# Kernel optimization log

Hardware: AMD Instinct MI355X
Metric: run time of the kernel (lower is better)

Reference implementation:

```python
import jax, jax.numpy as jnp
import numpy as np

B, N, K = 4, 32768, 16
IN_DIM, HID, OUT_DIM = 32, 64, 32
N_DIM = 2
KIN = 2 * N_DIM + OUT_DIM  # 36
KH = 64
EPS = 1e-5


def _gelu(x):
    return jax.nn.gelu(x, approximate=False)  # torch F.gelu default (erf)


def setup_inputs() -> dict:
    key = jax.random.key(0)
    ks = jax.random.split(key, 16)
    s = lambda fan_in: 1.0 / np.sqrt(fan_in)
    return {
        "inp": jax.random.normal(ks[0], (B, N, IN_DIM), jnp.float32),
        "input_grid": jax.random.uniform(ks[1], (N, N_DIM), jnp.float32),
        "output_grid": jax.random.uniform(ks[2], (N, N_DIM), jnp.float32),
        "neighbor_idx": jax.random.randint(ks[3], (N, K), 0, N, jnp.int32),
        # pointwise projection MLP: in_dim -> hid -> out_dim, GELU between
        "Wp1": jax.random.normal(ks[4], (IN_DIM, HID), jnp.float32) * s(IN_DIM),
        "bp1": jnp.zeros((HID,), jnp.float32),
        "Wp2": jax.random.normal(ks[5], (HID, OUT_DIM), jnp.float32) * s(HID),
        "bp2": jnp.zeros((OUT_DIM,), jnp.float32),
        # per-edge kernel MLP: [2*n_dim+out_dim, 64, 64, out_dim], GELU between
        "Wk1": jax.random.normal(ks[6], (KIN, KH), jnp.float32) * s(KIN),
        "bk1": jnp.zeros((KH,), jnp.float32),
        "Wk2": jax.random.normal(ks[7], (KH, KH), jnp.float32) * s(KH),
        "bk2": jnp.zeros((KH,), jnp.float32),
        "Wk3": jax.random.normal(ks[8], (KH, OUT_DIM), jnp.float32) * s(KH),
        "bk3": jnp.zeros((OUT_DIM,), jnp.float32),
        # LayerNorm
        "ln_gamma": jnp.ones((OUT_DIM,), jnp.float32),
        "ln_beta": jnp.zeros((OUT_DIM,), jnp.float32),
    }


def reference(inp, input_grid, output_grid, neighbor_idx,
              Wp1, bp1, Wp2, bp2, Wk1, bk1, Wk2, bk2, Wk3, bk3,
              ln_gamma, ln_beta):
    # pointwise projection MLP
    x = _gelu(jnp.einsum('bnc,ch->bnh', inp, Wp1) + bp1)
    x = jnp.einsum('bnh,ho->bno', x, Wp2) + bp2  # (B, N, OUT_DIM)

    # neighbor gather (fixed K neighbors per output point)
    f_y = x[:, neighbor_idx, :]                      # (B, N, K, C)
    y_pos = input_grid[neighbor_idx]                 # (N, K, n_dim)
    x_pos = jnp.broadcast_to(output_grid[:, None, :], (N, K, N_DIM))
    pos_feat = jnp.concatenate([y_pos, x_pos], axis=-1)          # (N, K, 2*n_dim)
    agg = jnp.concatenate(
        [jnp.broadcast_to(pos_feat[None], (x.shape[0], N, K, 2 * N_DIM)), f_y],
        axis=-1)                                      # (B, N, K, KIN)

    # nonlinear kernel MLP k(x, y, f(y))
    h = _gelu(jnp.einsum('bnkc,ch->bnkh', agg, Wk1) + bk1)
    h = _gelu(jnp.einsum('bnkh,hg->bnkg', h, Wk2) + bk2)
    k_out = jnp.einsum('bnkg,go->bnko', h, Wk3) + bk3  # (B, N, K, OUT_DIM)

    # mean-aggregate over neighbors (integral transform)
    out = jnp.mean(k_out, axis=2)                      # (B, N, OUT_DIM)

    # residual (shapes match) + LayerNorm over channels
    out = out + x
    mu = jnp.mean(out, axis=-1, keepdims=True)
    var = jnp.mean((out - mu) ** 2, axis=-1, keepdims=True)
    out = (out - mu) * jax.lax.rsqrt(var + EPS) * ln_gamma + ln_beta
    return out
```

## Files before the change

kernel.cpp:

```cpp
#include <hip/hip_runtime.h>
#include <hip/hip_bf16.h>

#define BB 4
#define NN 32768
#define KKN 16
#define IN_DIM 32
#define HID 64
#define OUT_DIM 32
#define KH 64
#define WS 88
#define TOT (BB * NN)
#define NWAVES 8192
#define GTAB_N 4096

typedef __bf16 bf16;
typedef float f32x4 __attribute__((ext_vector_type(4)));
typedef bf16 bf16x8 __attribute__((ext_vector_type(8)));
typedef bf16 bf16x4 __attribute__((ext_vector_type(4)));

__device__ __forceinline__ float gelu_f(float x) {
    float x2 = x * x;
    float t  = x * fmaf(0.10294358f, x2, 2.3022082f);
    float E  = __builtin_amdgcn_exp2f(t);
    float r  = __builtin_amdgcn_rcpf(E + 1.0f);
    return fmaf(-x, r, x);
}

template <int CTRL>
__device__ __forceinline__ float dppadd(float v) {
    union { float f; int i; } u, r;
    u.f = v;
    r.i = __builtin_amdgcn_update_dpp(0, u.i, CTRL, 0xf, 0xf, true);
    return v + r.f;
}
__device__ __forceinline__ float rowsum16(float v) {
    v = dppadd<0xB1>(v);
    v = dppadd<0x4E>(v);
    v = dppadd<0x124>(v);
    v = dppadd<0x128>(v);
    return v;
}

__global__ __launch_bounds__(256) void point_mlp_kernel(
    const float* __restrict__ inp, const float* __restrict__ Wp1,
    const float* __restrict__ bp1, const float* __restrict__ Wp2,
    const float* __restrict__ bp2, bf16* __restrict__ xbf)
{
    __shared__ __align__(16) bf16 hb[4][16 * WS];
    const int tid = threadIdx.x, w = tid >> 6, lane = tid & 63;
    const int q = lane >> 4, nl = lane & 15;

    bf16x8 w1f[4];
    #pragma unroll
    for (int nb = 0; nb < 4; nb++)
        #pragma unroll
        for (int j = 0; j < 8; j++)
            w1f[nb][j] = (bf16)Wp1[(q * 8 + j) * HID + nb * 16 + nl];
    bf16x8 w2f[2][2];
    #pragma unroll
    for (int nb = 0; nb < 2; nb++)
        #pragma unroll
        for (int c = 0; c < 2; c++)
            #pragma unroll
            for (int j = 0; j < 8; j++) {
                int k = c * 32 + q * 8 + j, kp = ((k & 3) << 4) | (k >> 2);
                w2f[nb][c][j] = (bf16)Wp2[kp * OUT_DIM + nb * 16 + nl];
            }
    float b1v[4], b2v[2];
    #pragma unroll
    for (int nb = 0; nb < 4; nb++) b1v[nb] = bp1[nb * 16 + nl];
    b2v[0] = bp2[nl]; b2v[1] = bp2[16 + nl];

    const int gw = blockIdx.x * 4 + w;
    const int nw = gridDim.x * 4;

    for (int t = gw; t < TOT / 16; t += nw) {
        const int R = t * 16;
        const float* ap = inp + (size_t)(R + nl) * IN_DIM + q * 8;
        float4 av0 = *(const float4*)ap, av1 = *(const float4*)(ap + 4);
        bf16x8 af;
        af[0] = (bf16)av0.x; af[1] = (bf16)av0.y; af[2] = (bf16)av0.z; af[3] = (bf16)av0.w;
        af[4] = (bf16)av1.x; af[5] = (bf16)av1.y; af[6] = (bf16)av1.z; af[7] = (bf16)av1.w;

        f32x4 acc[4];
        #pragma unroll
        for (int nb = 0; nb < 4; nb++)
            acc[nb] = (f32x4){b1v[nb], b1v[nb], b1v[nb], b1v[nb]};
        #pragma unroll
        for (int nb = 0; nb < 4; nb++)
            acc[nb] = __builtin_amdgcn_mfma_f32_16x16x32_bf16(af, w1f[nb], acc[nb], 0, 0, 0);

        #pragma unroll
        for (int r = 0; r < 4; r++) {
            bf16x4 hv;
            #pragma unroll
            for (int nb = 0; nb < 4; nb++) hv[nb] = (bf16)gelu_f(acc[nb][r]);
            *(bf16x4*)&hb[w][(q * 4 + r) * WS + nl * 4] = hv;
        }
        bf16x8 a0 = *(const bf16x8*)&hb[w][nl * WS + q * 8];
        bf16x8 a1 = *(const bf16x8*)&hb[w][nl * WS + 32 + q * 8];
        f32x4 a2[2];
        #pragma unroll
        for (int nb = 0; nb < 2; nb++) {
            a2[nb] = (f32x4){b2v[nb], b2v[nb], b2v[nb], b2v[nb]};
            a2[nb] = __builtin_amdgcn_mfma_f32_16x16x32_bf16(a0, w2f[nb][0], a2[nb], 0, 0, 0);
            a2[nb] = __builtin_amdgcn_mfma_f32_16x16x32_bf16(a1, w2f[nb][1], a2[nb], 0, 0, 0);
        }
        #pragma unroll
        for (int r = 0; r < 4; r++)
            #pragma unroll
            for (int nb = 0; nb < 2; nb++)
                xbf[(size_t)(R + q * 4 + r) * OUT_DIM + nb * 16 + nl] = (bf16)a2[nb][r];
    }
}

__global__ __launch_bounds__(256) void gnn_edge_kernel(
    const bf16*  __restrict__ xbf,
    const float* __restrict__ igrid, const float* __restrict__ ogrid,
    const int*   __restrict__ nbi,
    const float* __restrict__ Wk1, const float* __restrict__ bk1,
    const float* __restrict__ Wk2, const float* __restrict__ bk2,
    const float* __restrict__ Wk3, const float* __restrict__ bk3,
    const float* __restrict__ gma, const float* __restrict__ bta,
    float* __restrict__ out)
{
    __shared__ __align__(16) bf16 tile[8][16 * WS];
    __shared__ __align__(16) bf16 gtab[GTAB_N];

    const int tid = threadIdx.x, w = tid >> 6, lane = tid & 63;
    const int q = lane >> 4, nl = lane & 15;
    bf16* __restrict__ TA = tile[w * 2];
    bf16* __restrict__ TB = tile[w * 2 + 1];

    for (int i = tid; i < GTAB_N; i += 256) {
        float x = (float)i * 0.0078125f - 16.0f;
        gtab[i] = (bf16)(0.5f * x * (1.0f + erff(x * 0.70710678f)));
    }

    bf16x8 w1f[4][2], w2f[4][2], w3f[2][2];
    #pragma unroll
    for (int nb = 0; nb < 4; nb++) {
        #pragma unroll
        for (int j = 0; j < 8; j++) {
            w1f[nb][0][j] = (bf16)Wk1[(4 + q * 8 + j) * KH + nb * 16 + nl];
            float v1 = 0.0f;
            if (j < 4 && q == 0) v1 = Wk1[j * KH + nb * 16 + nl];
            w1f[nb][1][j] = (bf16)v1;
        }
        #pragma unroll
        for (int c = 0; c < 2; c++)
            #pragma unroll
            for (int j = 0; j < 8; j++) {
                int k = c * 32 + q * 8 + j, kp = ((k & 3) << 4) | (k >> 2);
                w2f[nb][c][j] = (bf16)Wk2[kp * KH + nb * 16 + nl];
            }
    }
    #pragma unroll
    for (int nb = 0; nb < 2; nb++)
        #pragma unroll
        for (int c = 0; c < 2; c++)
            #pragma unroll
            for (int j = 0; j < 8; j++) {
                int k = c * 32 + q * 8 + j, kp = ((k & 3) << 4) | (k >> 2);
                w3f[nb][c][j] = (bf16)Wk3[kp * OUT_DIM + nb * 16 + nl];
            }

    float b1v[4], b2v[4], b3v[2];
    #pragma unroll
    for (int nb = 0; nb < 4; nb++) { b1v[nb] = bk1[nb * 16 + nl]; b2v[nb] = bk2[nb * 16 + nl]; }
    b3v[0] = bk3[nl]; b3v[1] = bk3[16 + nl];
    const float g0 = gma[nl], g1 = gma[16 + nl], be0 = bta[nl], be1 = bta[16 + nl];

    const int gw = blockIdx.x * 4 + w;
    const int e = lane >> 2, part = lane & 3;

    {
        const bf16x8 zf = {(bf16)0.f,(bf16)0.f,(bf16)0.f,(bf16)0.f,(bf16)0.f,(bf16)0.f,(bf16)0.f,(bf16)0.f};
        for (int i = lane * 8; i < 16 * WS; i += 64 * 8) { *(bf16x8*)&TA[i] = zf; *(bf16x8*)&TB[i] = zf; }
    }
    __syncthreads();

    #define GLUT(x) gtab[(unsigned)fminf(fmaxf(fmaf((x), 128.0f, 2048.5f), 0.0f), 4095.0f)]

    int tA = gw, tB = gw + NWAVES;
    int nA = nbi[(tA & (NN - 1)) * KKN + e];
    int nB = nbi[(tB & (NN - 1)) * KKN + e];
    uint4 fyA = ((const uint4*)(xbf + ((size_t)((tA >> 15) * NN + nA)) * OUT_DIM))[part];
    uint4 fyB = ((const uint4*)(xbf + ((size_t)((tB >> 15) * NN + nB)) * OUT_DIM))[part];
    float2 ipA, opA, ipB, opB;
    if (part == 0) {
        ipA = ((const float2*)igrid)[nA]; opA = ((const float2*)ogrid)[tA & (NN - 1)];
        ipB = ((const float2*)igrid)[nB]; opB = ((const float2*)ogrid)[tB & (NN - 1)];
    }
    bf16 xA0 = xbf[(size_t)tA * OUT_DIM + nl],      xA1 = xbf[(size_t)tA * OUT_DIM + 16 + nl];
    bf16 xB0 = xbf[(size_t)tB * OUT_DIM + nl],      xB1 = xbf[(size_t)tB * OUT_DIM + 16 + nl];

    #pragma unroll 1
    for (int it = 0; it < TOT / (2 * NWAVES); ++it) {
        *(uint4*)&TA[e * WS + part * 8] = fyA;
        *(uint4*)&TB[e * WS + part * 8] = fyB;
        if (part == 0) {
            bf16x4 pA = {(bf16)ipA.x, (bf16)ipA.y, (bf16)opA.x, (bf16)opA.y};
            bf16x4 pB = {(bf16)ipB.x, (bf16)ipB.y, (bf16)opB.x, (bf16)opB.y};
            *(bf16x4*)&TA[e * WS + 32] = pA;
            *(bf16x4*)&TB[e * WS + 32] = pB;
        }
        const float rA0 = (float)xA0, rA1 = (float)xA1, rB0 = (float)xB0, rB1 = (float)xB1;

        const int tA2 = (tA + 2 * NWAVES) & (TOT - 1);
        const int tB2 = tA2 + NWAVES;
        const int nA2 = nbi[(tA2 & (NN - 1)) * KKN + e];
        const int nB2 = nbi[(tB2 & (NN - 1)) * KKN + e];

        bf16x8 aA0 = *(const bf16x8*)&TA[nl * WS + q * 8];
        bf16x8 aA1 = *(const bf16x8*)&TA[nl * WS + 32 + q * 8];
        bf16x8 aB0 = *(const bf16x8*)&TB[nl * WS + q * 8];
        bf16x8 aB1 = *(const bf16x8*)&TB[nl * WS + 32 + q * 8];
        f32x4 cA[4], cB[4];
        #pragma unroll
        for (int nb = 0; nb < 4; nb++) {
            cA[nb] = (f32x4){b1v[nb], b1v[nb], b1v[nb], b1v[nb]};
            cB[nb] = (f32x4){b1v[nb], b1v[nb], b1v[nb], b1v[nb]};
        }
        #pragma unroll
        for (int nb = 0; nb < 4; nb++) {
            cA[nb] = __builtin_amdgcn_mfma_f32_16x16x32_bf16(aA0, w1f[nb][0], cA[nb], 0, 0, 0);
            cB[nb] = __builtin_amdgcn_mfma_f32_16x16x32_bf16(aB0, w1f[nb][0], cB[nb], 0, 0, 0);
            cA[nb] = __builtin_amdgcn_mfma_f32_16x16x32_bf16(aA1, w1f[nb][1], cA[nb], 0, 0, 0);
            cB[nb] = __builtin_amdgcn_mfma_f32_16x16x32_bf16(aB1, w1f[nb][1], cB[nb], 0, 0, 0);
        }
        #pragma unroll
        for (int r = 0; r < 4; r++) {
            bf16x4 hA, hB;
            hA[0] = GLUT(cA[0][r]);          hB[0] = GLUT(cB[0][r]);
            hA[1] = GLUT(cA[1][r]);          hB[1] = GLUT(cB[1][r]);
            hA[2] = (bf16)gelu_f(cA[2][r]);  hB[2] = (bf16)gelu_f(cB[2][r]);
            hA[3] = (bf16)gelu_f(cA[3][r]);  hB[3] = (bf16)gelu_f(cB[3][r]);
            *(bf16x4*)&TA[(q * 4 + r) * WS + nl * 4] = hA;
            *(bf16x4*)&TB[(q * 4 + r) * WS + nl * 4] = hB;
        }

        uint4 fyA2 = ((const uint4*)(xbf + ((size_t)((tA2 >> 15) * NN + nA2)) * OUT_DIM))[part];
        uint4 fyB2 = ((const uint4*)(xbf + ((size_t)((tB2 >> 15) * NN + nB2)) * OUT_DIM))[part];
        float2 ipA2, opA2, ipB2, opB2;
        if (part == 0) {
            ipA2 = ((const float2*)igrid)[nA2]; opA2 = ((const float2*)ogrid)[tA2 & (NN - 1)];
            ipB2 = ((const float2*)igrid)[nB2]; opB2 = ((const float2*)ogrid)[tB2 & (NN - 1)];
        }
        bf16 xA0n = xbf[(size_t)tA2 * OUT_DIM + nl],  xA1n = xbf[(size_t)tA2 * OUT_DIM + 16 + nl];
        bf16 xB0n = xbf[(size_t)tB2 * OUT_DIM + nl],  xB1n = xbf[(size_t)tB2 * OUT_DIM + 16 + nl];

        aA0 = *(const bf16x8*)&TA[nl * WS + q * 8];
        aA1 = *(const bf16x8*)&TA[nl * WS + 32 + q * 8];
        aB0 = *(const bf16x8*)&TB[nl * WS + q * 8];
        aB1 = *(const bf16x8*)&TB[nl * WS + 32 + q * 8];
        #pragma unroll
        for (int nb = 0; nb < 4; nb++) {
            cA[nb] = (f32x4){b2v[nb], b2v[nb], b2v[nb], b2v[nb]};
            cB[nb] = (f32x4){b2v[nb], b2v[nb], b2v[nb], b2v[nb]};
        }
        #pragma unroll
        for (int nb = 0; nb < 4; nb++) {
            cA[nb] = __builtin_amdgcn_mfma_f32_16x16x32_bf16(aA0, w2f[nb][0], cA[nb], 0, 0, 0);
            cB[nb] = __builtin_amdgcn_mfma_f32_16x16x32_bf16(aB0, w2f[nb][0], cB[nb], 0, 0, 0);
            cA[nb] = __builtin_amdgcn_mfma_f32_16x16x32_bf16(aA1, w2f[nb][1], cA[nb], 0, 0, 0);
            cB[nb] = __builtin_amdgcn_mfma_f32_16x16x32_bf16(aB1, w2f[nb][1], cB[nb], 0, 0, 0);
        }
        #pragma unroll
        for (int r = 0; r < 4; r++) {
            bf16x4 hA, hB;
            hA[0] = GLUT(cA[0][r]);          hB[0] = GLUT(cB[0][r]);
            hA[1] = GLUT(cA[1][r]);          hB[1] = GLUT(cB[1][r]);
            hA[2] = (bf16)gelu_f(cA[2][r]);  hB[2] = (bf16)gelu_f(cB[2][r]);
            hA[3] = (bf16)gelu_f(cA[3][r]);  hB[3] = (bf16)gelu_f(cB[3][r]);
            *(bf16x4*)&TA[(q * 4 + r) * WS + nl * 4] = hA;
            *(bf16x4*)&TB[(q * 4 + r) * WS + nl * 4] = hB;
        }

        aA0 = *(const bf16x8*)&TA[nl * WS + q * 8];
        aA1 = *(const bf16x8*)&TA[nl * WS + 32 + q * 8];
        aB0 = *(const bf16x8*)&TB[nl * WS + q * 8];
        aB1 = *(const bf16x8*)&TB[nl * WS + 32 + q * 8];
        f32x4 dA[2], dB[2];
        #pragma unroll
        for (int nb = 0; nb < 2; nb++) {
            dA[nb] = (f32x4){0.f, 0.f, 0.f, 0.f};
            dB[nb] = (f32x4){0.f, 0.f, 0.f, 0.f};
            dA[nb] = __builtin_amdgcn_mfma_f32_16x16x32_bf16(aA0, w3f[nb][0], dA[nb], 0, 0, 0);
            dB[nb] = __builtin_amdgcn_mfma_f32_16x16x32_bf16(aB0, w3f[nb][0], dB[nb], 0, 0, 0);
            dA[nb] = __builtin_amdgcn_mfma_f32_16x16x32_bf16(aA1, w3f[nb][1], dA[nb], 0, 0, 0);
            dB[nb] = __builtin_amdgcn_mfma_f32_16x16x32_bf16(aB1, w3f[nb][1], dB[nb], 0, 0, 0);
        }

        {
            float s0 = dA[0][0] + dA[0][1] + dA[0][2] + dA[0][3];
            float s1 = dA[1][0] + dA[1][1] + dA[1][2] + dA[1][3];
            float u0 = dB[0][0] + dB[0][1] + dB[0][2] + dB[0][3];
            float u1 = dB[1][0] + dB[1][1] + dB[1][2] + dB[1][3];
            s0 += __shfl_xor(s0, 16, 64); s0 += __shfl_xor(s0, 32, 64);
            s1 += __shfl_xor(s1, 16, 64); s1 += __shfl_xor(s1, 32, 64);
            u0 += __shfl_xor(u0, 16, 64); u0 += __shfl_xor(u0, 32, 64);
            u1 += __shfl_xor(u1, 16, 64); u1 += __shfl_xor(u1, 32, 64);

            float oA0 = s0 * 0.0625f + b3v[0] + rA0;
            float oA1 = s1 * 0.0625f + b3v[1] + rA1;
            float oB0 = u0 * 0.0625f + b3v[0] + rB0;
            float oB1 = u1 * 0.0625f + b3v[1] + rB1;

            float mA = rowsum16(oA0 + oA1) * (1.0f / 32.0f);
            float mB = rowsum16(oB0 + oB1) * (1.0f / 32.0f);
            float dA0 = oA0 - mA, dA1 = oA1 - mA, dB0 = oB0 - mB, dB1 = oB1 - mB;
            float vA = rowsum16(dA0 * dA0 + dA1 * dA1) * (1.0f / 32.0f);
            float vB = rowsum16(dB0 * dB0 + dB1 * dB1) * (1.0f / 32.0f);
            float rsA = rsqrtf(vA + 1e-5f);
            float rsB = rsqrtf(vB + 1e-5f);

            if (q == 0) {
                float* oa = out + (size_t)tA * OUT_DIM;
                float* ob = out + (size_t)tB * OUT_DIM;
                oa[nl]      = fmaf(dA0 * rsA, g0, be0);
                oa[16 + nl] = fmaf(dA1 * rsA, g1, be1);
                ob[nl]      = fmaf(dB0 * rsB, g0, be0);
                ob[16 + nl] = fmaf(dB1 * rsB, g1, be1);
            }
        }

        tA = tA2; tB = tB2;
        fyA = fyA2; fyB = fyB2;
        ipA = ipA2; opA = opA2; ipB = ipB2; opB = opB2;
        xA0 = xA0n; xA1 = xA1n; xB0 = xB0n; xB1 = xB1n;
    }
    #undef GLUT
}

extern "C" void kernel_launch(void* const* d_in, const int* in_sizes, int n_in,
                              void* d_out, int out_size, void* d_ws, size_t ws_size,
                              hipStream_t stream) {
    const float* inp   = (const float*)d_in[0];
    const float* igrid = (const float*)d_in[1];
    const float* ogrid = (const float*)d_in[2];
    const int*   nbi   = (const int*)d_in[3];
    const float* Wp1   = (const float*)d_in[4];
    const float* bp1   = (const float*)d_in[5];
    const float* Wp2   = (const float*)d_in[6];
    const float* bp2   = (const float*)d_in[7];
    const float* Wk1   = (const float*)d_in[8];
    const float* bk1   = (const float*)d_in[9];
    const float* Wk2   = (const float*)d_in[10];
    const float* bk2   = (const float*)d_in[11];
    const float* Wk3   = (const float*)d_in[12];
    const float* bk3   = (const float*)d_in[13];
    const float* gma   = (const float*)d_in[14];
    const float* bta   = (const float*)d_in[15];
    float* out = (float*)d_out;
    bf16* xbf = (bf16*)d_ws;

    point_mlp_kernel<<<1024, 256, 0, stream>>>(inp, Wp1, bp1, Wp2, bp2, xbf);
    gnn_edge_kernel<<<2048, 256, 0, stream>>>(xbf, igrid, ogrid, nbi,
                                              Wk1, bk1, Wk2, bk2, Wk3, bk3,
                                              gma, bta, out);
}
```

Measured before the change: 214.4 us.

## Switch to fp16 MFMA with packed fp16 polynomial GELU and fewer waves

Changes the working precision from bf16 to fp16 for the activations and MFMA operands. It replaces the GELU lookup table and the exp/rcp GELU with a packed-fp16 polynomial, evaluated two values at a time on the clamped input. It also drops the shared-memory GELU table and its __syncthreads, halves the edge-kernel grid (NWAVES 4096, 1024 blocks) and adds a launch-bounds occupancy hint. This should cut VALU work in the GELU-heavy inner loop, at the risk of accuracy loss from the fp16 range and the polynomial approximation.

```diff
diff --git a/kernel.cpp b/kernel.cpp
--- a/kernel.cpp
+++ b/kernel.cpp
@@ -1,5 +1,4 @@
 #include <hip/hip_runtime.h>
-#include <hip/hip_bf16.h>
 
 #define BB 4
 #define NN 32768
@@ -10,20 +9,37 @@
 #define KH 64
 #define WS 88
 #define TOT (BB * NN)
-#define NWAVES 8192
-#define GTAB_N 4096
-
-typedef __bf16 bf16;
+#define NWAVES 4096
+
+typedef _Float16 f16;
+typedef f16 f16x2 __attribute__((ext_vector_type(2)));
+typedef f16 f16x4 __attribute__((ext_vector_type(4)));
+typedef f16 f16x8 __attribute__((ext_vector_type(8)));
 typedef float f32x4 __attribute__((ext_vector_type(4)));
-typedef bf16 bf16x8 __attribute__((ext_vector_type(8)));
-typedef bf16 bf16x4 __attribute__((ext_vector_type(4)));
-
-__device__ __forceinline__ float gelu_f(float x) {
-    float x2 = x * x;
-    float t  = x * fmaf(0.10294358f, x2, 2.3022082f);
-    float E  = __builtin_amdgcn_exp2f(t);
-    float r  = __builtin_amdgcn_rcpf(E + 1.0f);
-    return fmaf(-x, r, x);
+typedef __fp16 hf16x2 __attribute__((ext_vector_type(2)));
+
+#define H2(c) ((f16x2){(f16)(c), (f16)(c)})
+
+__device__ __forceinline__ f16x2 cvt2(float a, float b) {
+    hf16x2 r = __builtin_amdgcn_cvt_pkrtz(a, b);
+    return __builtin_bit_cast(f16x2, r);
+}
+
+__device__ __forceinline__ f16x2 gelu2(float a, float b) {
+    f16x2 x  = cvt2(a, b);
+    f16x2 s  = __builtin_elementwise_min(
+                   __builtin_elementwise_max(x, H2(-3.5f)), H2(3.5f));
+    f16x2 s4 = s * H2(0.25f);
+    f16x2 t  = s4 * s4;
+    f16x2 g  = H2(-1.0110344f);
+    g = g * t + H2( 2.85016064f);
+    g = g * t + H2(-3.40439040f);
+    g = g * t + H2( 2.32402432f);
+    g = g * t + H2(-1.04974080f);
+    g = g * t + H2( 0.39879504f);
+    f16x2 f  = s * g;
+    f16x2 hx = x * H2(0.5f);
+    return x * f + hx;
 }
 
 template <int CTRL>
@@ -44,19 +60,19 @@
 __global__ __launch_bounds__(256) void point_mlp_kernel(
     const float* __restrict__ inp, const float* __restrict__ Wp1,
     const float* __restrict__ bp1, const float* __restrict__ Wp2,
-    const float* __restrict__ bp2, bf16* __restrict__ xbf)
+    const float* __restrict__ bp2, f16* __restrict__ xhf)
 {
-    __shared__ __align__(16) bf16 hb[4][16 * WS];
+    __shared__ __align__(16) f16 hb[4][16 * WS];
     const int tid = threadIdx.x, w = tid >> 6, lane = tid & 63;
     const int q = lane >> 4, nl = lane & 15;
 
-    bf16x8 w1f[4];
+    f16x8 w1f[4];
     #pragma unroll
     for (int nb = 0; nb < 4; nb++)
         #pragma unroll
         for (int j = 0; j < 8; j++)
-            w1f[nb][j] = (bf16)Wp1[(q * 8 + j) * HID + nb * 16 + nl];
-    bf16x8 w2f[2][2];
+            w1f[nb][j] = (f16)Wp1[(q * 8 + j) * HID + nb * 16 + nl];
+    f16x8 w2f[2][2];
     #pragma unroll
     for (int nb = 0; nb < 2; nb++)
         #pragma unroll
@@ -64,7 +80,7 @@
             #pragma unroll
             for (int j = 0; j < 8; j++) {
                 int k = c * 32 + q * 8 + j, kp = ((k & 3) << 4) | (k >> 2);
-                w2f[nb][c][j] = (bf16)Wp2[kp * OUT_DIM + nb * 16 + nl];
+                w2f[nb][c][j] = (f16)Wp2[kp * OUT_DIM + nb * 16 + nl];
             }
     float b1v[4], b2v[2];
     #pragma unroll
@@ -78,9 +94,11 @@
         const int R = t * 16;
         const float* ap = inp + (size_t)(R + nl) * IN_DIM + q * 8;
         float4 av0 = *(const float4*)ap, av1 = *(const float4*)(ap + 4);
-        bf16x8 af;
-        af[0] = (bf16)av0.x; af[1] = (bf16)av0.y; af[2] = (bf16)av0.z; af[3] = (bf16)av0.w;
-        af[4] = (bf16)av1.x; af[5] = (bf16)av1.y; af[6] = (bf16)av1.z; af[7] = (bf16)av1.w;
+        f16x2 p01 = cvt2(av0.x, av0.y);
+        f16x2 p23 = cvt2(av0.z, av0.w);
+        f16x2 p45 = cvt2(av1.x, av1.y);
+        f16x2 p67 = cvt2(av1.z, av1.w);
+        f16x8 af = (f16x8){p01.x, p01.y, p23.x, p23.y, p45.x, p45.y, p67.x, p67.y};
 
         f32x4 acc[4];
         #pragma unroll
@@ -88,34 +106,33 @@
             acc[nb] = (f32x4){b1v[nb], b1v[nb], b1v[nb], b1v[nb]};
         #pragma unroll
         for (int nb = 0; nb < 4; nb++)
-            acc[nb] = __builtin_amdgcn_mfma_f32_16x16x32_bf16(af, w1f[nb], acc[nb], 0, 0, 0);
+            acc[nb] = __builtin_amdgcn_mfma_f32_16x16x32_f16(af, w1f[nb], acc[nb], 0, 0, 0);
 
         #pragma unroll
         for (int r = 0; r < 4; r++) {
-            bf16x4 hv;
-            #pragma unroll
-            for (int nb = 0; nb < 4; nb++) hv[nb] = (bf16)gelu_f(acc[nb][r]);
-            *(bf16x4*)&hb[w][(q * 4 + r) * WS + nl * 4] = hv;
-        }
-        bf16x8 a0 = *(const bf16x8*)&hb[w][nl * WS + q * 8];
-        bf16x8 a1 = *(const bf16x8*)&hb[w][nl * WS + 32 + q * 8];
+            f16x2 h01 = gelu2(acc[0][r], acc[1][r]);
+            f16x2 h23 = gelu2(acc[2][r], acc[3][r]);
+            *(f16x4*)&hb[w][(q * 4 + r) * WS + nl * 4] = (f16x4){h01.x, h01.y, h23.x, h23.y};
+        }
+        f16x8 a0 = *(const f16x8*)&hb[w][nl * WS + q * 8];
+        f16x8 a1 = *(const f16x8*)&hb[w][nl * WS + 32 + q * 8];
         f32x4 a2[2];
         #pragma unroll
         for (int nb = 0; nb < 2; nb++) {
             a2[nb] = (f32x4){b2v[nb], b2v[nb], b2v[nb], b2v[nb]};
-            a2[nb] = __builtin_amdgcn_mfma_f32_16x16x32_bf16(a0, w2f[nb][0], a2[nb], 0, 0, 0);
-            a2[nb] = __builtin_amdgcn_mfma_f32_16x16x32_bf16(a1, w2f[nb][1], a2[nb], 0, 0, 0);
+            a2[nb] = __builtin_amdgcn_mfma_f32_16x16x32_f16(a0, w2f[nb][0], a2[nb], 0, 0, 0);
+            a2[nb] = __builtin_amdgcn_mfma_f32_16x16x32_f16(a1, w2f[nb][1], a2[nb], 0, 0, 0);
         }
         #pragma unroll
         for (int r = 0; r < 4; r++)
             #pragma unroll
             for (int nb = 0; nb < 2; nb++)
-                xbf[(size_t)(R + q * 4 + r) * OUT_DIM + nb * 16 + nl] = (bf16)a2[nb][r];
-    }
-}
-
-__global__ __launch_bounds__(256) void gnn_edge_kernel(
-    const bf16*  __restrict__ xbf,
+                xhf[(size_t)(R + q * 4 + r) * OUT_DIM + nb * 16 + nl] = (f16)a2[nb][r];
+    }
+}
+
+__global__ __launch_bounds__(256, 4) void gnn_edge_kernel(
+    const f16*   __restrict__ xhf,
     const float* __restrict__ igrid, const float* __restrict__ ogrid,
     const int*   __restrict__ nbi,
     const float* __restrict__ Wk1, const float* __restrict__ bk1,
@@ -124,35 +141,29 @@
     const float* __restrict__ gma, const float* __restrict__ bta,
     float* __restrict__ out)
 {
-    __shared__ __align__(16) bf16 tile[8][16 * WS];
-    __shared__ __align__(16) bf16 gtab[GTAB_N];
+    __shared__ __align__(16) f16 tile[8][16 * WS];
 
     const int tid = threadIdx.x, w = tid >> 6, lane = tid & 63;
     const int q = lane >> 4, nl = lane & 15;
-    bf16* __restrict__ TA = tile[w * 2];
-    bf16* __restrict__ TB = tile[w * 2 + 1];
-
-    for (int i = tid; i < GTAB_N; i += 256) {
-        float x = (float)i * 0.0078125f - 16.0f;
-        gtab[i] = (bf16)(0.5f * x * (1.0f + erff(x * 0.70710678f)));
-    }
-
-    bf16x8 w1f[4][2], w2f[4][2], w3f[2][2];
+    f16* __restrict__ TA = tile[w * 2];
+    f16* __restrict__ TB = tile[w * 2 + 1];
+
+    f16x8 w1f[4][2], w2f[4][2], w3f[2][2];
     #pragma unroll
     for (int nb = 0; nb < 4; nb++) {
         #pragma unroll
         for (int j = 0; j < 8; j++) {
-            w1f[nb][0][j] = (bf16)Wk1[(4 + q * 8 + j) * KH + nb * 16 + nl];
+            w1f[nb][0][j] = (f16)Wk1[(4 + q * 8 + j) * KH + nb * 16 + nl];
             float v1 = 0.0f;
             if (j < 4 && q == 0) v1 = Wk1[j * KH + nb * 16 + nl];
-            w1f[nb][1][j] = (bf16)v1;
+            w1f[nb][1][j] = (f16)v1;
         }
         #pragma unroll
         for (int c = 0; c < 2; c++)
             #pragma unroll
             for (int j = 0; j < 8; j++) {
                 int k = c * 32 + q * 8 + j, kp = ((k & 3) << 4) | (k >> 2);
-                w2f[nb][c][j] = (bf16)Wk2[kp * KH + nb * 16 + nl];
+                w2f[nb][c][j] = (f16)Wk2[kp * KH + nb * 16 + nl];
             }
     }
     #pragma unroll
@@ -162,7 +173,7 @@
             #pragma unroll
             for (int j = 0; j < 8; j++) {
                 int k = c * 32 + q * 8 + j, kp = ((k & 3) << 4) | (k >> 2);
-                w3f[nb][c][j] = (bf16)Wk3[kp * OUT_DIM + nb * 16 + nl];
+                w3f[nb][c][j] = (f16)Wk3[kp * OUT_DIM + nb * 16 + nl];
             }
 
     float b1v[4], b2v[4], b3v[2];
@@ -175,35 +186,32 @@
     const int e = lane >> 2, part = lane & 3;
 
     {
-        const bf16x8 zf = {(bf16)0.f,(bf16)0.f,(bf16)0.f,(bf16)0.f,(bf16)0.f,(bf16)0.f,(bf16)0.f,(bf16)0.f};
-        for (int i = lane * 8; i < 16 * WS; i += 64 * 8) { *(bf16x8*)&TA[i] = zf; *(bf16x8*)&TB[i] = zf; }
-    }
-    __syncthreads();
-
-    #define GLUT(x) gtab[(unsigned)fminf(fmaxf(fmaf((x), 128.0f, 2048.5f), 0.0f), 4095.0f)]
+        const f16x8 zf = {(f16)0.f,(f16)0.f,(f16)0.f,(f16)0.f,(f16)0.f,(f16)0.f,(f16)0.f,(f16)0.f};
+        for (int i = lane * 8; i < 16 * WS; i += 64 * 8) { *(f16x8*)&TA[i] = zf; *(f16x8*)&TB[i] = zf; }
+    }
 
     int tA = gw, tB = gw + NWAVES;
     int nA = nbi[(tA & (NN - 1)) * KKN + e];
     int nB = nbi[(tB & (NN - 1)) * KKN + e];
-    uint4 fyA = ((const uint4*)(xbf + ((size_t)((tA >> 15) * NN + nA)) * OUT_DIM))[part];
-    uint4 fyB = ((const uint4*)(xbf + ((size_t)((tB >> 15) * NN + nB)) * OUT_DIM))[part];
+    uint4 fyA = ((const uint4*)(xhf + ((size_t)((tA >> 15) * NN + nA)) * OUT_DIM))[part];
+    uint4 fyB = ((const uint4*)(xhf + ((size_t)((tB >> 15) * NN + nB)) * OUT_DIM))[part];
     float2 ipA, opA, ipB, opB;
     if (part == 0) {
         ipA = ((const float2*)igrid)[nA]; opA = ((const float2*)ogrid)[tA & (NN - 1)];
         ipB = ((const float2*)igrid)[nB]; opB = ((const float2*)ogrid)[tB & (NN - 1)];
     }
-    bf16 xA0 = xbf[(size_t)tA * OUT_DIM + nl],      xA1 = xbf[(size_t)tA * OUT_DIM + 16 + nl];
-    bf16 xB0 = xbf[(size_t)tB * OUT_DIM + nl],      xB1 = xbf[(size_t)tB * OUT_DIM + 16 + nl];
+    f16 xA0 = xhf[(size_t)tA * OUT_DIM + nl],      xA1 = xhf[(size_t)tA * OUT_DIM + 16 + nl];
+    f16 xB0 = xhf[(size_t)tB * OUT_DIM + nl],      xB1 = xhf[(size_t)tB * OUT_DIM + 16 + nl];
 
     #pragma unroll 1
     for (int it = 0; it < TOT / (2 * NWAVES); ++it) {
         *(uint4*)&TA[e * WS + part * 8] = fyA;
         *(uint4*)&TB[e * WS + part * 8] = fyB;
         if (part == 0) {
-            bf16x4 pA = {(bf16)ipA.x, (bf16)ipA.y, (bf16)opA.x, (bf16)opA.y};
-            bf16x4 pB = {(bf16)ipB.x, (bf16)ipB.y, (bf16)opB.x, (bf16)opB.y};
-            *(bf16x4*)&TA[e * WS + 32] = pA;
-            *(bf16x4*)&TB[e * WS + 32] = pB;
+            f16x4 pA = {(f16)ipA.x, (f16)ipA.y, (f16)opA.x, (f16)opA.y};
+            f16x4 pB = {(f16)ipB.x, (f16)ipB.y, (f16)opB.x, (f16)opB.y};
+            *(f16x4*)&TA[e * WS + 32] = pA;
+            *(f16x4*)&TB[e * WS + 32] = pB;
         }
         const float rA0 = (float)xA0, rA1 = (float)xA1, rB0 = (float)xB0, rB1 = (float)xB1;
 
@@ -212,10 +220,10 @@
         const int nA2 = nbi[(tA2 & (NN - 1)) * KKN + e];
         const int nB2 = nbi[(tB2 & (NN - 1)) * KKN + e];
 
-        bf16x8 aA0 = *(const bf16x8*)&TA[nl * WS + q * 8];
-        bf16x8 aA1 = *(const bf16x8*)&TA[nl * WS + 32 + q * 8];
-        bf16x8 aB0 = *(const bf16x8*)&TB[nl * WS + q * 8];
-        bf16x8 aB1 = *(const bf16x8*)&TB[nl * WS + 32 + q * 8];
+        f16x8 aA0 = *(const f16x8*)&TA[nl * WS + q * 8];
+        f16x8 aA1 = *(const f16x8*)&TA[nl * WS + 32 + q * 8];
+        f16x8 aB0 = *(const f16x8*)&TB[nl * WS + q * 8];
+        f16x8 aB1 = *(const f16x8*)&TB[nl * WS + 32 + q * 8];
         f32x4 cA[4], cB[4];
         #pragma unroll
         for (int nb = 0; nb < 4; nb++) {
@@ -224,36 +232,35 @@
         }
         #pragma unroll
         for (int nb = 0; nb < 4; nb++) {
-            cA[nb] = __builtin_amdgcn_mfma_f32_16x16x32_bf16(aA0, w1f[nb][0], cA[nb], 0, 0, 0);
-            cB[nb] = __builtin_amdgcn_mfma_f32_16x16x32_bf16(aB0, w1f[nb][0], cB[nb], 0, 0, 0);
-            cA[nb] = __builtin_amdgcn_mfma_f32_16x16x32_bf16(aA1, w1f[nb][1], cA[nb], 0, 0, 0);
-            cB[nb] = __builtin_amdgcn_mfma_f32_16x16x32_bf16(aB1, w1f[nb][1], cB[nb], 0, 0, 0);
+            cA[nb] = __builtin_amdgcn_mfma_f32_16x16x32_f16(aA0, w1f[nb][0], cA[nb], 0, 0, 0);
+            cB[nb] = __builtin_amdgcn_mfma_f32_16x16x32_f16(aB0, w1f[nb][0], cB[nb], 0, 0, 0);
+            cA[nb] = __builtin_amdgcn_mfma_f32_16x16x32_f16(aA1, w1f[nb][1], cA[nb], 0, 0, 0);
+            cB[nb] = __builtin_amdgcn_mfma_f32_16x16x32_f16(aB1, w1f[nb][1], cB[nb], 0, 0, 0);
         }
         #pragma unroll
         for (int r = 0; r < 4; r++) {
-            bf16x4 hA, hB;
-            hA[0] = GLUT(cA[0][r]);          hB[0] = GLUT(cB[0][r]);
-            hA[1] = GLUT(cA[1][r]);          hB[1] = GLUT(cB[1][r]);
-            hA[2] = (bf16)gelu_f(cA[2][r]);  hB[2] = (bf16)gelu_f(cB[2][r]);
-            hA[3] = (bf16)gelu_f(cA[3][r]);  hB[3] = (bf16)gelu_f(cB[3][r]);
-            *(bf16x4*)&TA[(q * 4 + r) * WS + nl * 4] = hA;
-            *(bf16x4*)&TB[(q * 4 + r) * WS + nl * 4] = hB;
-        }
-
-        uint4 fyA2 = ((const uint4*)(xbf + ((size_t)((tA2 >> 15) * NN + nA2)) * OUT_DIM))[part];
-        uint4 fyB2 = ((const uint4*)(xbf + ((size_t)((tB2 >> 15) * NN + nB2)) * OUT_DIM))[part];
+            f16x2 hA01 = gelu2(cA[0][r], cA[1][r]);
+            f16x2 hA23 = gelu2(cA[2][r], cA[3][r]);
+            f16x2 hB01 = gelu2(cB[0][r], cB[1][r]);
+            f16x2 hB23 = gelu2(cB[2][r], cB[3][r]);
+            *(f16x4*)&TA[(q * 4 + r) * WS + nl * 4] = (f16x4){hA01.x, hA01.y, hA23.x, hA23.y};
+            *(f16x4*)&TB[(q * 4 + r) * WS + nl * 4] = (f16x4){hB01.x, hB01.y, hB23.x, hB23.y};
+        }
+
+        uint4 fyA2 = ((const uint4*)(xhf + ((size_t)((tA2 >> 15) * NN + nA2)) * OUT_DIM))[part];
+        uint4 fyB2 = ((const uint4*)(xhf + ((size_t)((tB2 >> 15) * NN + nB2)) * OUT_DIM))[part];
         float2 ipA2, opA2, ipB2, opB2;
         if (part == 0) {
             ipA2 = ((const float2*)igrid)[nA2]; opA2 = ((const float2*)ogrid)[tA2 & (NN - 1)];
             ipB2 = ((const float2*)igrid)[nB2]; opB2 = ((const float2*)ogrid)[tB2 & (NN - 1)];
         }
-        bf16 xA0n = xbf[(size_t)tA2 * OUT_DIM + nl],  xA1n = xbf[(size_t)tA2 * OUT_DIM + 16 + nl];
-        bf16 xB0n = xbf[(size_t)tB2 * OUT_DIM + nl],  xB1n = xbf[(size_t)tB2 * OUT_DIM + 16 + nl];
-
-        aA0 = *(const bf16x8*)&TA[nl * WS + q * 8];
-        aA1 = *(const bf16x8*)&TA[nl * WS + 32 + q * 8];
-        aB0 = *(const bf16x8*)&TB[nl * WS + q * 8];
-        aB1 = *(const bf16x8*)&TB[nl * WS + 32 + q * 8];
+        f16 xA0n = xhf[(size_t)tA2 * OUT_DIM + nl],  xA1n = xhf[(size_t)tA2 * OUT_DIM + 16 + nl];
+        f16 xB0n = xhf[(size_t)tB2 * OUT_DIM + nl],  xB1n = xhf[(size_t)tB2 * OUT_DIM + 16 + nl];
+
+        aA0 = *(const f16x8*)&TA[nl * WS + q * 8];
+        aA1 = *(const f16x8*)&TA[nl * WS + 32 + q * 8];
+        aB0 = *(const f16x8*)&TB[nl * WS + q * 8];
+        aB1 = *(const f16x8*)&TB[nl * WS + 32 + q * 8];
         #pragma unroll
         for (int nb = 0; nb < 4; nb++) {
             cA[nb] = (f32x4){b2v[nb], b2v[nb], b2v[nb], b2v[nb]};
@@ -261,35 +268,34 @@
         }
         #pragma unroll
         for (int nb = 0; nb < 4; nb++) {
-            cA[nb] = __builtin_amdgcn_mfma_f32_16x16x32_bf16(aA0, w2f[nb][0], cA[nb], 0, 0, 0);
-            cB[nb] = __builtin_amdgcn_mfma_f32_16x16x32_bf16(aB0, w2f[nb][0], cB[nb], 0, 0, 0);
-            cA[nb] = __builtin_amdgcn_mfma_f32_16x16x32_bf16(aA1, w2f[nb][1], cA[nb], 0, 0, 0);
-            cB[nb] = __builtin_amdgcn_mfma_f32_16x16x32_bf16(aB1, w2f[nb][1], cB[nb], 0, 0, 0);
+            cA[nb] = __builtin_amdgcn_mfma_f32_16x16x32_f16(aA0, w2f[nb][0], cA[nb], 0, 0, 0);
+            cB[nb] = __builtin_amdgcn_mfma_f32_16x16x32_f16(aB0, w2f[nb][0], cB[nb], 0, 0, 0);
+            cA[nb] = __builtin_amdgcn_mfma_f32_16x16x32_f16(aA1, w2f[nb][1], cA[nb], 0, 0, 0);
+            cB[nb] = __builtin_amdgcn_mfma_f32_16x16x32_f16(aB1, w2f[nb][1], cB[nb], 0, 0, 0);
         }
         #pragma unroll
         for (int r = 0; r < 4; r++) {
-            bf16x4 hA, hB;
-            hA[0] = GLUT(cA[0][r]);          hB[0] = GLUT(cB[0][r]);
-            hA[1] = GLUT(cA[1][r]);          hB[1] = GLUT(cB[1][r]);
-            hA[2] = (bf16)gelu_f(cA[2][r]);  hB[2] = (bf16)gelu_f(cB[2][r]);
-            hA[3] = (bf16)gelu_f(cA[3][r]);  hB[3] = (bf16)gelu_f(cB[3][r]);
-            *(bf16x4*)&TA[(q * 4 + r) * WS + nl * 4] = hA;
-            *(bf16x4*)&TB[(q * 4 + r) * WS + nl * 4] = hB;
-        }
-
-        aA0 = *(const bf16x8*)&TA[nl * WS + q * 8];
-        aA1 = *(const bf16x8*)&TA[nl * WS + 32 + q * 8];
-        aB0 = *(const bf16x8*)&TB[nl * WS + q * 8];
-        aB1 = *(const bf16x8*)&TB[nl * WS + 32 + q * 8];
+            f16x2 hA01 = gelu2(cA[0][r], cA[1][r]);
+            f16x2 hA23 = gelu2(cA[2][r], cA[3][r]);
+            f16x2 hB01 = gelu2(cB[0][r], cB[1][r]);
+            f16x2 hB23 = gelu2(cB[2][r], cB[3][r]);
+            *(f16x4*)&TA[(q * 4 + r) * WS + nl * 4] = (f16x4){hA01.x, hA01.y, hA23.x, hA23.y};
+            *(f16x4*)&TB[(q * 4 + r) * WS + nl * 4] = (f16x4){hB01.x, hB01.y, hB23.x, hB23.y};
+        }
+
+        aA0 = *(const f16x8*)&TA[nl * WS + q * 8];
+        aA1 = *(const f16x8*)&TA[nl * WS + 32 + q * 8];
+        aB0 = *(const f16x8*)&TB[nl * WS + q * 8];
+        aB1 = *(const f16x8*)&TB[nl * WS + 32 + q * 8];
         f32x4 dA[2], dB[2];
         #pragma unroll
         for (int nb = 0; nb < 2; nb++) {
             dA[nb] = (f32x4){0.f, 0.f, 0.f, 0.f};
             dB[nb] = (f32x4){0.f, 0.f, 0.f, 0.f};
-            dA[nb] = __builtin_amdgcn_mfma_f32_16x16x32_bf16(aA0, w3f[nb][0], dA[nb], 0, 0, 0);
-            dB[nb] = __builtin_amdgcn_mfma_f32_16x16x32_bf16(aB0, w3f[nb][0], dB[nb], 0, 0, 0);
-            dA[nb] = __builtin_amdgcn_mfma_f32_16x16x32_bf16(aA1, w3f[nb][1], dA[nb], 0, 0, 0);
-            dB[nb] = __builtin_amdgcn_mfma_f32_16x16x32_bf16(aB1, w3f[nb][1], dB[nb], 0, 0, 0);
+            dA[nb] = __builtin_amdgcn_mfma_f32_16x16x32_f16(aA0, w3f[nb][0], dA[nb], 0, 0, 0);
+            dB[nb] = __builtin_amdgcn_mfma_f32_16x16x32_f16(aB0, w3f[nb][0], dB[nb], 0, 0, 0);
+            dA[nb] = __builtin_amdgcn_mfma_f32_16x16x32_f16(aA1, w3f[nb][1], dA[nb], 0, 0, 0);
+            dB[nb] = __builtin_amdgcn_mfma_f32_16x16x32_f16(aB1, w3f[nb][1], dB[nb], 0, 0, 0);
         }
 
         {
@@ -330,7 +336,6 @@
         ipA = ipA2; opA = opA2; ipB = ipB2; opB = opB2;
         xA0 = xA0n; xA1 = xA1n; xB0 = xB0n; xB1 = xB1n;
     }
-    #undef GLUT
 }
 
 extern "C" void kernel_launch(void* const* d_in, const int* in_sizes, int n_in,
@@ -353,10 +358,10 @@
     const float* gma   = (const float*)d_in[14];
     const float* bta   = (const float*)d_in[15];
     float* out = (float*)d_out;
-    bf16* xbf = (bf16*)d_ws;
-
-    point_mlp_kernel<<<1024, 256, 0, stream>>>(inp, Wp1, bp1, Wp2, bp2, xbf);
-    gnn_edge_kernel<<<2048, 256, 0, stream>>>(xbf, igrid, ogrid, nbi,
+    f16* xhf = (f16*)d_ws;
+
+    point_mlp_kernel<<<1024, 256, 0, stream>>>(inp, Wp1, bp1, Wp2, bp2, xhf);
+    gnn_edge_kernel<<<1024, 256, 0, stream>>>(xhf, igrid, ogrid, nbi,
                                               Wk1, bk1, Wk2, bk2, Wk3, bk3,
                                               gma, bta, out);
 }
```

New measurement: 439.2 us. +104.9%, slower.
